# Kernel optimization log

Hardware: AMD Instinct MI355X
Metric: run time of the kernel (lower is better)

The kernel has to match this reference:

```python
import jax, jax.numpy as jnp
import numpy as np

N_NODES = 100000
N_EDGES = 1600000
D_FEAT = 64


def setup_inputs() -> dict:
    key = jax.random.key(0)
    k1, k2, k3, k4 = jax.random.split(key, 4)
    rows = jnp.sort(jax.random.randint(k1, (N_EDGES,), 0, N_NODES, dtype=jnp.int64))
    cols = jax.random.randint(k2, (N_EDGES,), 0, N_NODES, dtype=jnp.int64)
    vals = jax.random.uniform(k3, (N_EDGES,), dtype=jnp.float32)
    embeds = jax.random.normal(k4, (N_NODES, D_FEAT), dtype=jnp.float32)
    return {"rows": rows, "cols": cols, "vals": vals, "embeds": embeds}


def reference(rows, cols, vals, embeds):
    # out[i] = sum_{e: rows[e]==i} vals[e] * embeds[cols[e]]  (torch.spmm with COO adj)
    gathered = vals[:, None] * embeds[cols]          # [E, d]
    out = jax.ops.segment_sum(gathered, rows, num_segments=N_NODES)  # [N, d]
    return out
```

## Files before the change

### kernel.cpp

```cpp
#include <hip/hip_runtime.h>
#include <hip/hip_bf16.h>


constexpr int D = 64;

__device__ __forceinline__ unsigned bf16rnd(unsigned u) {
    return (u + 0x7FFFu + ((u >> 16) & 1u)) >> 16;
}

__global__ __launch_bounds__(256) void prep_kernel(
    const uint4* __restrict__ src,
    uint4* __restrict__ dst,
    int n8,
    const int* __restrict__ rows, int* __restrict__ row_ptr,
    int n_edges, int n_nodes, int cvt_blocks)
{
    if ((int)blockIdx.x < cvt_blocks) {
        int i = blockIdx.x * 256 + threadIdx.x;
        if (i >= n8) return;
        uint4 a = src[2 * i];
        uint4 b = src[2 * i + 1];
        uint4 o;
        o.x = bf16rnd(a.x) | (bf16rnd(a.y) << 16);
        o.y = bf16rnd(a.z) | (bf16rnd(a.w) << 16);
        o.z = bf16rnd(b.x) | (bf16rnd(b.y) << 16);
        o.w = bf16rnd(b.z) | (bf16rnd(b.w) << 16);
        dst[i] = o;
    } else {
        int e = (blockIdx.x - cvt_blocks) * 256 + threadIdx.x;
        if (e >= n_edges) return;
        int r_cur  = rows[e];
        int r_prev = (e == 0) ? -1 : rows[e - 1];
        for (int r = r_prev + 1; r <= r_cur; ++r) row_ptr[r] = e;
        if (e == n_edges - 1)
            for (int r = r_cur + 1; r <= n_nodes; ++r) row_ptr[r] = n_edges;
    }
}

__device__ __forceinline__ float bflo(unsigned w) {
    union { unsigned u; float f; } x; x.u = w << 16; return x.f;
}
__device__ __forceinline__ float bfhi(unsigned w) {
    union { unsigned u; float f; } x; x.u = w & 0xFFFF0000u; return x.f;
}

__global__ __launch_bounds__(256, 4) void spmm_node_kernel(
    const int* __restrict__ row_ptr,
    const int* __restrict__ cols,
    const float* __restrict__ vals,
    const uint4* __restrict__ ebf4,
    float4* __restrict__ out4,
    int n_nodes)
{
    constexpr int CHUNK = 256;
    __shared__ int   s_cols[4][CHUNK];
    __shared__ float s_vals[4][CHUNK];

    const int lane = threadIdx.x & 63;
    const int t    = lane & 7;
    const int s    = lane >> 3;
    const int w    = threadIdx.x >> 6;
    const int wave = blockIdx.x * (blockDim.x >> 6) + w;
    const int node = wave * 8 + s;
    if (node >= n_nodes) return;

    const int nb    = wave * 8;
    const int nbhi  = (nb + 8 <= n_nodes) ? nb + 8 : n_nodes;
    const int wbase = row_ptr[nb];
    const int wend  = row_ptr[nbhi];
    const int lo    = row_ptr[node];
    const int hi    = row_ptr[node + 1];

    float4 acc0 = make_float4(0.f, 0.f, 0.f, 0.f);
    float4 acc1 = make_float4(0.f, 0.f, 0.f, 0.f);

    for (int cbase = wbase; cbase < wend; cbase += CHUNK) {
        #pragma unroll
        for (int j = 0; j < CHUNK; j += 64) {
            if (cbase + j >= wend) break;
            int idx = cbase + j + lane;
            if (idx < wend) {
                s_cols[w][j + lane] = cols[idx];
                s_vals[w][j + lane] = vals[idx];
            }
        }
        __builtin_amdgcn_wave_barrier();

        const int cend = (cbase + CHUNK < wend) ? cbase + CHUNK : wend;
        int e0 = (lo > cbase) ? lo : cbase;
        int e1 = (hi < cend)  ? hi : cend;

        for (int e = e0; e < e1; e += 8) {
            const int last = e1 - 1;
            int i0 = e - cbase;
            int i1 = ((e + 1 <= last) ? e + 1 : last) - cbase;
            int i2 = ((e + 2 <= last) ? e + 2 : last) - cbase;
            int i3 = ((e + 3 <= last) ? e + 3 : last) - cbase;
            int i4 = ((e + 4 <= last) ? e + 4 : last) - cbase;
            int i5 = ((e + 5 <= last) ? e + 5 : last) - cbase;
            int i6 = ((e + 6 <= last) ? e + 6 : last) - cbase;
            int i7 = ((e + 7 <= last) ? e + 7 : last) - cbase;

            int c0 = s_cols[w][i0], c1 = s_cols[w][i1];
            int c2 = s_cols[w][i2], c3 = s_cols[w][i3];
            int c4 = s_cols[w][i4], c5 = s_cols[w][i5];
            int c6 = s_cols[w][i6], c7 = s_cols[w][i7];

            float v0 = s_vals[w][i0];
            float v1 = (e + 1 < e1) ? s_vals[w][i1] : 0.f;
            float v2 = (e + 2 < e1) ? s_vals[w][i2] : 0.f;
            float v3 = (e + 3 < e1) ? s_vals[w][i3] : 0.f;
            float v4 = (e + 4 < e1) ? s_vals[w][i4] : 0.f;
            float v5 = (e + 5 < e1) ? s_vals[w][i5] : 0.f;
            float v6 = (e + 6 < e1) ? s_vals[w][i6] : 0.f;
            float v7 = (e + 7 < e1) ? s_vals[w][i7] : 0.f;

            uint4 m0 = ebf4[c0 * 8 + t];
            uint4 m1 = ebf4[c1 * 8 + t];
            uint4 m2 = ebf4[c2 * 8 + t];
            uint4 m3 = ebf4[c3 * 8 + t];
            uint4 m4 = ebf4[c4 * 8 + t];
            uint4 m5 = ebf4[c5 * 8 + t];
            uint4 m6 = ebf4[c6 * 8 + t];
            uint4 m7 = ebf4[c7 * 8 + t];

            acc0.x += v0 * bflo(m0.x); acc0.y += v0 * bfhi(m0.x);
            acc0.z += v0 * bflo(m0.y); acc0.w += v0 * bfhi(m0.y);
            acc1.x += v0 * bflo(m0.z); acc1.y += v0 * bfhi(m0.z);
            acc1.z += v0 * bflo(m0.w); acc1.w += v0 * bfhi(m0.w);

            acc0.x += v1 * bflo(m1.x); acc0.y += v1 * bfhi(m1.x);
            acc0.z += v1 * bflo(m1.y); acc0.w += v1 * bfhi(m1.y);
            acc1.x += v1 * bflo(m1.z); acc1.y += v1 * bfhi(m1.z);
            acc1.z += v1 * bflo(m1.w); acc1.w += v1 * bfhi(m1.w);

            acc0.x += v2 * bflo(m2.x); acc0.y += v2 * bfhi(m2.x);
            acc0.z += v2 * bflo(m2.y); acc0.w += v2 * bfhi(m2.y);
            acc1.x += v2 * bflo(m2.z); acc1.y += v2 * bfhi(m2.z);
            acc1.z += v2 * bflo(m2.w); acc1.w += v2 * bfhi(m2.w);

            acc0.x += v3 * bflo(m3.x); acc0.y += v3 * bfhi(m3.x);
            acc0.z += v3 * bflo(m3.y); acc0.w += v3 * bfhi(m3.y);
            acc1.x += v3 * bflo(m3.z); acc1.y += v3 * bfhi(m3.z);
            acc1.z += v3 * bflo(m3.w); acc1.w += v3 * bfhi(m3.w);

            acc0.x += v4 * bflo(m4.x); acc0.y += v4 * bfhi(m4.x);
            acc0.z += v4 * bflo(m4.y); acc0.w += v4 * bfhi(m4.y);
            acc1.x += v4 * bflo(m4.z); acc1.y += v4 * bfhi(m4.z);
            acc1.z += v4 * bflo(m4.w); acc1.w += v4 * bfhi(m4.w);

            acc0.x += v5 * bflo(m5.x); acc0.y += v5 * bfhi(m5.x);
            acc0.z += v5 * bflo(m5.y); acc0.w += v5 * bfhi(m5.y);
            acc1.x += v5 * bflo(m5.z); acc1.y += v5 * bfhi(m5.z);
            acc1.z += v5 * bflo(m5.w); acc1.w += v5 * bfhi(m5.w);

            acc0.x += v6 * bflo(m6.x); acc0.y += v6 * bfhi(m6.x);
            acc0.z += v6 * bflo(m6.y); acc0.w += v6 * bfhi(m6.y);
            acc1.x += v6 * bflo(m6.z); acc1.y += v6 * bfhi(m6.z);
            acc1.z += v6 * bflo(m6.w); acc1.w += v6 * bfhi(m6.w);

            acc0.x += v7 * bflo(m7.x); acc0.y += v7 * bfhi(m7.x);
            acc0.z += v7 * bflo(m7.y); acc0.w += v7 * bfhi(m7.y);
            acc1.x += v7 * bflo(m7.z); acc1.y += v7 * bfhi(m7.z);
            acc1.z += v7 * bflo(m7.w); acc1.w += v7 * bfhi(m7.w);
        }
        __builtin_amdgcn_wave_barrier();
    }

    long ob = (long)node * 16 + 2 * t;
    out4[ob]     = acc0;
    out4[ob + 1] = acc1;
}

extern "C" void kernel_launch(void* const* d_in, const int* in_sizes, int n_in,
                              void* d_out, int out_size, void* d_ws, size_t ws_size,
                              hipStream_t stream) {
    const int*   rows   = (const int*)d_in[0];
    const int*   cols   = (const int*)d_in[1];
    const float* vals   = (const float*)d_in[2];
    const float* embeds = (const float*)d_in[3];
    float4*      out4   = (float4*)d_out;

    const int n_edges = in_sizes[0];
    const int n_nodes = out_size / D;
    const int n_feat  = in_sizes[3];

    char*  ws        = (char*)d_ws;
    uint4* ebf_table = (uint4*)ws;
    int*   row_ptr   = (int*)(ws + (size_t)n_feat * 2);

    int n8         = n_feat / 8;
    int cvt_blocks = (n8 + 255) / 256;
    int row_blocks = (n_edges + 255) / 256;
    prep_kernel<<<cvt_blocks + row_blocks, 256, 0, stream>>>(
        (const uint4*)embeds, ebf_table, n8,
        rows, row_ptr, n_edges, n_nodes, cvt_blocks);

    int waves  = (n_nodes + 7) / 8;
    int blocks = (waves + 3) / 4;
    spmm_node_kernel<<<blocks, 256, 0, stream>>>(
        row_ptr, cols, vals, ebf_table, out4, n_nodes);
}
```

Baseline: 119.6 us.

## Fuse prep and SpMM into one cooperative persistent kernel with grid sync

Merges the bf16 conversion / row_ptr build and the SpMM gather into a single cooperative kernel launched with 1024 persistent blocks, separated by a grid-wide sync, with grid-stride loops over node octets. This removes one kernel launch and the inter-kernel gap. It adds the cost of a grid barrier and a fixed grid size, and the fallback path keeps the old two-kernel launch. The fallback SpMM kernel's edge unroll is also cut from 8 to 4, which matters only if the cooperative launch fails.

```diff
diff --git a/kernel.cpp b/kernel.cpp
--- a/kernel.cpp
+++ b/kernel.cpp
@@ -1,5 +1,8 @@
 #include <hip/hip_runtime.h>
 #include <hip/hip_bf16.h>
+#include <hip/hip_cooperative_groups.h>
+
+namespace cg = cooperative_groups;
 
 
 constexpr int D = 64;
@@ -7,11 +10,173 @@
 __device__ __forceinline__ unsigned bf16rnd(unsigned u) {
     return (u + 0x7FFFu + ((u >> 16) & 1u)) >> 16;
 }
+__device__ __forceinline__ float bflo(unsigned w) {
+    union { unsigned u; float f; } x; x.u = w << 16; return x.f;
+}
+__device__ __forceinline__ float bfhi(unsigned w) {
+    union { unsigned u; float f; } x; x.u = w & 0xFFFF0000u; return x.f;
+}
+
+__global__ __launch_bounds__(256, 4) void fused_kernel(
+    const int* __restrict__ rows,
+    const int* __restrict__ cols,
+    const float* __restrict__ vals,
+    const uint4* __restrict__ src,
+    uint4* __restrict__ ebf4,
+    int* __restrict__ row_ptr,
+    float4* __restrict__ out4,
+    int n8, int n_edges, int n_nodes)
+{
+    const int tid  = blockIdx.x * 256 + threadIdx.x;
+    const int nthr = gridDim.x * 256;
+
+    for (int i = tid; i < n8; i += nthr) {
+        uint4 a = src[2 * i];
+        uint4 b = src[2 * i + 1];
+        uint4 o;
+        o.x = bf16rnd(a.x) | (bf16rnd(a.y) << 16);
+        o.y = bf16rnd(a.z) | (bf16rnd(a.w) << 16);
+        o.z = bf16rnd(b.x) | (bf16rnd(b.y) << 16);
+        o.w = bf16rnd(b.z) | (bf16rnd(b.w) << 16);
+        ebf4[i] = o;
+    }
+    for (int e = tid; e < n_edges; e += nthr) {
+        int r_cur  = rows[e];
+        int r_prev = (e == 0) ? -1 : rows[e - 1];
+        for (int r = r_prev + 1; r <= r_cur; ++r) row_ptr[r] = e;
+        if (e == n_edges - 1)
+            for (int r = r_cur + 1; r <= n_nodes; ++r) row_ptr[r] = n_edges;
+    }
+
+    cg::this_grid().sync();
+
+    constexpr int CHUNK = 256;
+    __shared__ int   s_cols[4][CHUNK];
+    __shared__ float s_vals[4][CHUNK];
+
+    const int lane   = threadIdx.x & 63;
+    const int t      = lane & 7;
+    const int s      = lane >> 3;
+    const int w      = threadIdx.x >> 6;
+    const int nwaves = gridDim.x * 4;
+    const int noct   = (n_nodes + 7) / 8;
+
+    for (int oct = blockIdx.x * 4 + w; oct < noct; oct += nwaves) {
+        const int nb    = oct * 8;
+        const int node  = nb + s;
+        const int nbhi  = (nb + 8 <= n_nodes) ? nb + 8 : n_nodes;
+        const int wbase = row_ptr[nb];
+        const int wend  = row_ptr[nbhi];
+        const bool live = (node < n_nodes);
+        const int lo    = live ? row_ptr[node]     : wend;
+        const int hi    = live ? row_ptr[node + 1] : wend;
+
+        float4 acc0 = make_float4(0.f, 0.f, 0.f, 0.f);
+        float4 acc1 = make_float4(0.f, 0.f, 0.f, 0.f);
+
+        for (int cbase = wbase; cbase < wend; cbase += CHUNK) {
+            #pragma unroll
+            for (int j = 0; j < CHUNK; j += 64) {
+                if (cbase + j >= wend) break;
+                int idx = cbase + j + lane;
+                if (idx < wend) {
+                    s_cols[w][j + lane] = cols[idx];
+                    s_vals[w][j + lane] = vals[idx];
+                }
+            }
+            __builtin_amdgcn_wave_barrier();
+
+            const int cend = (cbase + CHUNK < wend) ? cbase + CHUNK : wend;
+            int e0 = (lo > cbase) ? lo : cbase;
+            int e1 = (hi < cend)  ? hi : cend;
+
+            for (int e = e0; e < e1; e += 8) {
+                const int last = e1 - 1;
+                int i0 = e - cbase;
+                int i1 = ((e + 1 <= last) ? e + 1 : last) - cbase;
+                int i2 = ((e + 2 <= last) ? e + 2 : last) - cbase;
+                int i3 = ((e + 3 <= last) ? e + 3 : last) - cbase;
+                int i4 = ((e + 4 <= last) ? e + 4 : last) - cbase;
+                int i5 = ((e + 5 <= last) ? e + 5 : last) - cbase;
+                int i6 = ((e + 6 <= last) ? e + 6 : last) - cbase;
+                int i7 = ((e + 7 <= last) ? e + 7 : last) - cbase;
+
+                int c0 = s_cols[w][i0], c1 = s_cols[w][i1];
+                int c2 = s_cols[w][i2], c3 = s_cols[w][i3];
+                int c4 = s_cols[w][i4], c5 = s_cols[w][i5];
+                int c6 = s_cols[w][i6], c7 = s_cols[w][i7];
+
+                float v0 = s_vals[w][i0];
+                float v1 = (e + 1 < e1) ? s_vals[w][i1] : 0.f;
+                float v2 = (e + 2 < e1) ? s_vals[w][i2] : 0.f;
+                float v3 = (e + 3 < e1) ? s_vals[w][i3] : 0.f;
+                float v4 = (e + 4 < e1) ? s_vals[w][i4] : 0.f;
+                float v5 = (e + 5 < e1) ? s_vals[w][i5] : 0.f;
+                float v6 = (e + 6 < e1) ? s_vals[w][i6] : 0.f;
+                float v7 = (e + 7 < e1) ? s_vals[w][i7] : 0.f;
+
+                uint4 m0 = ebf4[c0 * 8 + t];
+                uint4 m1 = ebf4[c1 * 8 + t];
+                uint4 m2 = ebf4[c2 * 8 + t];
+                uint4 m3 = ebf4[c3 * 8 + t];
+                uint4 m4 = ebf4[c4 * 8 + t];
+                uint4 m5 = ebf4[c5 * 8 + t];
+                uint4 m6 = ebf4[c6 * 8 + t];
+                uint4 m7 = ebf4[c7 * 8 + t];
+
+                acc0.x += v0 * bflo(m0.x); acc0.y += v0 * bfhi(m0.x);
+                acc0.z += v0 * bflo(m0.y); acc0.w += v0 * bfhi(m0.y);
+                acc1.x += v0 * bflo(m0.z); acc1.y += v0 * bfhi(m0.z);
+                acc1.z += v0 * bflo(m0.w); acc1.w += v0 * bfhi(m0.w);
+
+                acc0.x += v1 * bflo(m1.x); acc0.y += v1 * bfhi(m1.x);
+                acc0.z += v1 * bflo(m1.y); acc0.w += v1 * bfhi(m1.y);
+                acc1.x += v1 * bflo(m1.z); acc1.y += v1 * bfhi(m1.z);
+                acc1.z += v1 * bflo(m1.w); acc1.w += v1 * bfhi(m1.w);
+
+                acc0.x += v2 * bflo(m2.x); acc0.y += v2 * bfhi(m2.x);
+                acc0.z += v2 * bflo(m2.y); acc0.w += v2 * bfhi(m2.y);
+                acc1.x += v2 * bflo(m2.z); acc1.y += v2 * bfhi(m2.z);
+                acc1.z += v2 * bflo(m2.w); acc1.w += v2 * bfhi(m2.w);
+
+                acc0.x += v3 * bflo(m3.x); acc0.y += v3 * bfhi(m3.x);
+                acc0.z += v3 * bflo(m3.y); acc0.w += v3 * bfhi(m3.y);
+                acc1.x += v3 * bflo(m3.z); acc1.y += v3 * bfhi(m3.z);
+                acc1.z += v3 * bflo(m3.w); acc1.w += v3 * bfhi(m3.w);
+
+                acc0.x += v4 * bflo(m4.x); acc0.y += v4 * bfhi(m4.x);
+                acc0.z += v4 * bflo(m4.y); acc0.w += v4 * bfhi(m4.y);
+                acc1.x += v4 * bflo(m4.z); acc1.y += v4 * bfhi(m4.z);
+                acc1.z += v4 * bflo(m4.w); acc1.w += v4 * bfhi(m4.w);
+
+                acc0.x += v5 * bflo(m5.x); acc0.y += v5 * bfhi(m5.x);
+                acc0.z += v5 * bflo(m5.y); acc0.w += v5 * bfhi(m5.y);
+                acc1.x += v5 * bflo(m5.z); acc1.y += v5 * bfhi(m5.z);
+                acc1.z += v5 * bflo(m5.w); acc1.w += v5 * bfhi(m5.w);
+
+                acc0.x += v6 * bflo(m6.x); acc0.y += v6 * bfhi(m6.x);
+                acc0.z += v6 * bflo(m6.y); acc0.w += v6 * bfhi(m6.y);
+                acc1.x += v6 * bflo(m6.z); acc1.y += v6 * bfhi(m6.z);
+                acc1.z += v6 * bflo(m6.w); acc1.w += v6 * bfhi(m6.w);
+
+                acc0.x += v7 * bflo(m7.x); acc0.y += v7 * bfhi(m7.x);
+                acc0.z += v7 * bflo(m7.y); acc0.w += v7 * bfhi(m7.y);
+                acc1.x += v7 * bflo(m7.z); acc1.y += v7 * bfhi(m7.z);
+                acc1.z += v7 * bflo(m7.w); acc1.w += v7 * bfhi(m7.w);
+            }
+            __builtin_amdgcn_wave_barrier();
+        }
+
+        if (live) {
+            long ob = (long)node * 16 + 2 * t;
+            out4[ob]     = acc0;
+            out4[ob + 1] = acc1;
+        }
+    }
+}
 
 __global__ __launch_bounds__(256) void prep_kernel(
-    const uint4* __restrict__ src,
-    uint4* __restrict__ dst,
-    int n8,
+    const uint4* __restrict__ src, uint4* __restrict__ dst, int n8,
     const int* __restrict__ rows, int* __restrict__ row_ptr,
     int n_edges, int n_nodes, int cvt_blocks)
 {
@@ -37,20 +202,10 @@
     }
 }
 
-__device__ __forceinline__ float bflo(unsigned w) {
-    union { unsigned u; float f; } x; x.u = w << 16; return x.f;
-}
-__device__ __forceinline__ float bfhi(unsigned w) {
-    union { unsigned u; float f; } x; x.u = w & 0xFFFF0000u; return x.f;
-}
-
 __global__ __launch_bounds__(256, 4) void spmm_node_kernel(
-    const int* __restrict__ row_ptr,
-    const int* __restrict__ cols,
-    const float* __restrict__ vals,
-    const uint4* __restrict__ ebf4,
-    float4* __restrict__ out4,
-    int n_nodes)
+    const int* __restrict__ row_ptr, const int* __restrict__ cols,
+    const float* __restrict__ vals, const uint4* __restrict__ ebf4,
+    float4* __restrict__ out4, int n_nodes)
 {
     constexpr int CHUNK = 256;
     __shared__ int   s_cols[4][CHUNK];
@@ -90,39 +245,24 @@
         int e0 = (lo > cbase) ? lo : cbase;
         int e1 = (hi < cend)  ? hi : cend;
 
-        for (int e = e0; e < e1; e += 8) {
+        for (int e = e0; e < e1; e += 4) {
             const int last = e1 - 1;
             int i0 = e - cbase;
             int i1 = ((e + 1 <= last) ? e + 1 : last) - cbase;
             int i2 = ((e + 2 <= last) ? e + 2 : last) - cbase;
             int i3 = ((e + 3 <= last) ? e + 3 : last) - cbase;
-            int i4 = ((e + 4 <= last) ? e + 4 : last) - cbase;
-            int i5 = ((e + 5 <= last) ? e + 5 : last) - cbase;
-            int i6 = ((e + 6 <= last) ? e + 6 : last) - cbase;
-            int i7 = ((e + 7 <= last) ? e + 7 : last) - cbase;
 
             int c0 = s_cols[w][i0], c1 = s_cols[w][i1];
             int c2 = s_cols[w][i2], c3 = s_cols[w][i3];
-            int c4 = s_cols[w][i4], c5 = s_cols[w][i5];
-            int c6 = s_cols[w][i6], c7 = s_cols[w][i7];
-
             float v0 = s_vals[w][i0];
             float v1 = (e + 1 < e1) ? s_vals[w][i1] : 0.f;
             float v2 = (e + 2 < e1) ? s_vals[w][i2] : 0.f;
             float v3 = (e + 3 < e1) ? s_vals[w][i3] : 0.f;
-            float v4 = (e + 4 < e1) ? s_vals[w][i4] : 0.f;
-            float v5 = (e + 5 < e1) ? s_vals[w][i5] : 0.f;
-            float v6 = (e + 6 < e1) ? s_vals[w][i6] : 0.f;
-            float v7 = (e + 7 < e1) ? s_vals[w][i7] : 0.f;
 
             uint4 m0 = ebf4[c0 * 8 + t];
             uint4 m1 = ebf4[c1 * 8 + t];
             uint4 m2 = ebf4[c2 * 8 + t];
             uint4 m3 = ebf4[c3 * 8 + t];
-            uint4 m4 = ebf4[c4 * 8 + t];
-            uint4 m5 = ebf4[c5 * 8 + t];
-            uint4 m6 = ebf4[c6 * 8 + t];
-            uint4 m7 = ebf4[c7 * 8 + t];
 
             acc0.x += v0 * bflo(m0.x); acc0.y += v0 * bfhi(m0.x);
             acc0.z += v0 * bflo(m0.y); acc0.w += v0 * bfhi(m0.y);
@@ -143,26 +283,6 @@
             acc0.z += v3 * bflo(m3.y); acc0.w += v3 * bfhi(m3.y);
             acc1.x += v3 * bflo(m3.z); acc1.y += v3 * bfhi(m3.z);
             acc1.z += v3 * bflo(m3.w); acc1.w += v3 * bfhi(m3.w);
-
-            acc0.x += v4 * bflo(m4.x); acc0.y += v4 * bfhi(m4.x);
-            acc0.z += v4 * bflo(m4.y); acc0.w += v4 * bfhi(m4.y);
-            acc1.x += v4 * bflo(m4.z); acc1.y += v4 * bfhi(m4.z);
-            acc1.z += v4 * bflo(m4.w); acc1.w += v4 * bfhi(m4.w);
-
-            acc0.x += v5 * bflo(m5.x); acc0.y += v5 * bfhi(m5.x);
-            acc0.z += v5 * bflo(m5.y); acc0.w += v5 * bfhi(m5.y);
-            acc1.x += v5 * bflo(m5.z); acc1.y += v5 * bfhi(m5.z);
-            acc1.z += v5 * bflo(m5.w); acc1.w += v5 * bfhi(m5.w);
-
-            acc0.x += v6 * bflo(m6.x); acc0.y += v6 * bfhi(m6.x);
-            acc0.z += v6 * bflo(m6.y); acc0.w += v6 * bfhi(m6.y);
-            acc1.x += v6 * bflo(m6.z); acc1.y += v6 * bfhi(m6.z);
-            acc1.z += v6 * bflo(m6.w); acc1.w += v6 * bfhi(m6.w);
-
-            acc0.x += v7 * bflo(m7.x); acc0.y += v7 * bfhi(m7.x);
-            acc0.z += v7 * bflo(m7.y); acc0.w += v7 * bfhi(m7.y);
-            acc1.x += v7 * bflo(m7.z); acc1.y += v7 * bfhi(m7.z);
-            acc1.z += v7 * bflo(m7.w); acc1.w += v7 * bfhi(m7.w);
         }
         __builtin_amdgcn_wave_barrier();
     }
@@ -189,15 +309,24 @@
     uint4* ebf_table = (uint4*)ws;
     int*   row_ptr   = (int*)(ws + (size_t)n_feat * 2);
 
-    int n8         = n_feat / 8;
-    int cvt_blocks = (n8 + 255) / 256;
-    int row_blocks = (n_edges + 255) / 256;
-    prep_kernel<<<cvt_blocks + row_blocks, 256, 0, stream>>>(
-        (const uint4*)embeds, ebf_table, n8,
-        rows, row_ptr, n_edges, n_nodes, cvt_blocks);
-
-    int waves  = (n_nodes + 7) / 8;
-    int blocks = (waves + 3) / 4;
-    spmm_node_kernel<<<blocks, 256, 0, stream>>>(
-        row_ptr, cols, vals, ebf_table, out4, n_nodes);
-}
+    int n8 = n_feat / 8;
+
+    const uint4* src = (const uint4*)embeds;
+    void* args[] = { (void*)&rows, (void*)&cols, (void*)&vals, (void*)&src,
+                     (void*)&ebf_table, (void*)&row_ptr, (void*)&out4,
+                     (void*)&n8, (void*)&n_edges, (void*)&n_nodes };
+
+    hipError_t err = hipLaunchCooperativeKernel(
+        (const void*)fused_kernel, dim3(1024), dim3(256), args, 0, stream);
+
+    if (err != hipSuccess) {
+        int cvt_blocks = (n8 + 255) / 256;
+        int row_blocks = (n_edges + 255) / 256;
+        prep_kernel<<<cvt_blocks + row_blocks, 256, 0, stream>>>(
+            src, ebf_table, n8, rows, row_ptr, n_edges, n_nodes, cvt_blocks);
+        int waves  = (n_nodes + 7) / 8;
+        int blocks = (waves + 3) / 4;
+        spmm_node_kernel<<<blocks, 256, 0, stream>>>(
+            row_ptr, cols, vals, ebf_table, out4, n_nodes);
+    }
+}
```

New measurement: 201.8 us. 68.7% more time.

## Replace row_ptr construction with per-wave binary search over sorted rows

Applied to the files above, without the earlier changes.

Drops the row-pointer build from the prep kernel, which previously read all 1.6M row indices and wrote the CSR offsets. Each wave now finds its segment boundaries with a parallel lower-bound binary search over the sorted rows array, one lane per boundary, and broadcasts the results with shuffles. Edge column/value loads and output stores also become nontemporal. The search costs about 21 dependent global loads per wave, which adds latency at wave start in exchange for removing the CSR-build pass and its memory traffic.

```diff
diff --git a/kernel.cpp b/kernel.cpp
--- a/kernel.cpp
+++ b/kernel.cpp
@@ -1,42 +1,13 @@
 #include <hip/hip_runtime.h>
-#include <hip/hip_bf16.h>
 
 
 constexpr int D = 64;
 
+typedef float v4f __attribute__((ext_vector_type(4)));
+
 __device__ __forceinline__ unsigned bf16rnd(unsigned u) {
     return (u + 0x7FFFu + ((u >> 16) & 1u)) >> 16;
 }
-
-__global__ __launch_bounds__(256) void prep_kernel(
-    const uint4* __restrict__ src,
-    uint4* __restrict__ dst,
-    int n8,
-    const int* __restrict__ rows, int* __restrict__ row_ptr,
-    int n_edges, int n_nodes, int cvt_blocks)
-{
-    if ((int)blockIdx.x < cvt_blocks) {
-        int i = blockIdx.x * 256 + threadIdx.x;
-        if (i >= n8) return;
-        uint4 a = src[2 * i];
-        uint4 b = src[2 * i + 1];
-        uint4 o;
-        o.x = bf16rnd(a.x) | (bf16rnd(a.y) << 16);
-        o.y = bf16rnd(a.z) | (bf16rnd(a.w) << 16);
-        o.z = bf16rnd(b.x) | (bf16rnd(b.y) << 16);
-        o.w = bf16rnd(b.z) | (bf16rnd(b.w) << 16);
-        dst[i] = o;
-    } else {
-        int e = (blockIdx.x - cvt_blocks) * 256 + threadIdx.x;
-        if (e >= n_edges) return;
-        int r_cur  = rows[e];
-        int r_prev = (e == 0) ? -1 : rows[e - 1];
-        for (int r = r_prev + 1; r <= r_cur; ++r) row_ptr[r] = e;
-        if (e == n_edges - 1)
-            for (int r = r_cur + 1; r <= n_nodes; ++r) row_ptr[r] = n_edges;
-    }
-}
-
 __device__ __forceinline__ float bflo(unsigned w) {
     union { unsigned u; float f; } x; x.u = w << 16; return x.f;
 }
@@ -44,13 +15,30 @@
     union { unsigned u; float f; } x; x.u = w & 0xFFFF0000u; return x.f;
 }
 
+__global__ __launch_bounds__(256) void prep_kernel(
+    const uint4* __restrict__ src,
+    uint4* __restrict__ dst,
+    int n8)
+{
+    int i = blockIdx.x * 256 + threadIdx.x;
+    if (i >= n8) return;
+    uint4 a = src[2 * i];
+    uint4 b = src[2 * i + 1];
+    uint4 o;
+    o.x = bf16rnd(a.x) | (bf16rnd(a.y) << 16);
+    o.y = bf16rnd(a.z) | (bf16rnd(a.w) << 16);
+    o.z = bf16rnd(b.x) | (bf16rnd(b.y) << 16);
+    o.w = bf16rnd(b.z) | (bf16rnd(b.w) << 16);
+    dst[i] = o;
+}
+
 __global__ __launch_bounds__(256, 4) void spmm_node_kernel(
-    const int* __restrict__ row_ptr,
+    const int* __restrict__ rows,
     const int* __restrict__ cols,
     const float* __restrict__ vals,
     const uint4* __restrict__ ebf4,
     float4* __restrict__ out4,
-    int n_nodes)
+    int n_edges, int n_nodes)
 {
     constexpr int CHUNK = 256;
     __shared__ int   s_cols[4][CHUNK];
@@ -60,16 +48,23 @@
     const int t    = lane & 7;
     const int s    = lane >> 3;
     const int w    = threadIdx.x >> 6;
-    const int wave = blockIdx.x * (blockDim.x >> 6) + w;
-    const int node = wave * 8 + s;
-    if (node >= n_nodes) return;
+    const int wave = blockIdx.x * 4 + w;
+    const int nb   = wave * 8;
+    if (nb >= n_nodes) return;
 
-    const int nb    = wave * 8;
-    const int nbhi  = (nb + 8 <= n_nodes) ? nb + 8 : n_nodes;
-    const int wbase = row_ptr[nb];
-    const int wend  = row_ptr[nbhi];
-    const int lo    = row_ptr[node];
-    const int hi    = row_ptr[node + 1];
+    int target = nb + (lane < 8 ? lane : 8);
+    if (target > n_nodes) target = n_nodes;
+    int sl = 0, sh = n_edges;
+    while (sl < sh) {
+        int mid = (sl + sh) >> 1;
+        if (rows[mid] < target) sl = mid + 1; else sh = mid;
+    }
+    const int wbase = __shfl(sl, 0);
+    const int wend  = __shfl(sl, 8);
+    const int lo    = __shfl(sl, s);
+    const int hi    = __shfl(sl, s + 1);
+    const int node  = nb + s;
+    const bool live = (node < n_nodes);
 
     float4 acc0 = make_float4(0.f, 0.f, 0.f, 0.f);
     float4 acc1 = make_float4(0.f, 0.f, 0.f, 0.f);
@@ -80,8 +75,8 @@
             if (cbase + j >= wend) break;
             int idx = cbase + j + lane;
             if (idx < wend) {
-                s_cols[w][j + lane] = cols[idx];
-                s_vals[w][j + lane] = vals[idx];
+                s_cols[w][j + lane] = __builtin_nontemporal_load(&cols[idx]);
+                s_vals[w][j + lane] = __builtin_nontemporal_load(&vals[idx]);
             }
         }
         __builtin_amdgcn_wave_barrier();
@@ -167,9 +162,11 @@
         __builtin_amdgcn_wave_barrier();
     }
 
-    long ob = (long)node * 16 + 2 * t;
-    out4[ob]     = acc0;
-    out4[ob + 1] = acc1;
+    if (live) {
+        long ob = (long)node * 16 + 2 * t;
+        __builtin_nontemporal_store(*(const v4f*)&acc0, (v4f*)&out4[ob]);
+        __builtin_nontemporal_store(*(const v4f*)&acc1, (v4f*)&out4[ob + 1]);
+    }
 }
 
 extern "C" void kernel_launch(void* const* d_in, const int* in_sizes, int n_in,
@@ -185,19 +182,14 @@
     const int n_nodes = out_size / D;
     const int n_feat  = in_sizes[3];
 
-    char*  ws        = (char*)d_ws;
-    uint4* ebf_table = (uint4*)ws;
-    int*   row_ptr   = (int*)(ws + (size_t)n_feat * 2);
+    uint4* ebf_table = (uint4*)d_ws;
 
     int n8         = n_feat / 8;
     int cvt_blocks = (n8 + 255) / 256;
-    int row_blocks = (n_edges + 255) / 256;
-    prep_kernel<<<cvt_blocks + row_blocks, 256, 0, stream>>>(
-        (const uint4*)embeds, ebf_table, n8,
-        rows, row_ptr, n_edges, n_nodes, cvt_blocks);
+    prep_kernel<<<cvt_blocks, 256, 0, stream>>>(
+        (const uint4*)embeds, ebf_table, n8);
 
-    int waves  = (n_nodes + 7) / 8;
-    int blocks = (waves + 3) / 4;
+    int blocks = (n_nodes + 31) / 32;
     spmm_node_kernel<<<blocks, 256, 0, stream>>>(
-        row_ptr, cols, vals, ebf_table, out4, n_nodes);
+        rows, cols, vals, ebf_table, out4, n_edges, n_nodes);
 }
```

Measured after the change: 129.8 us. 8.5% more time.
